# Kernel optimization log

Hardware: AMD Instinct MI355X
Metric: run time of the kernel (lower is better)

Reference implementation:

```python
import jax, jax.numpy as jnp
import numpy as np

NEG_SLOPE = 0.01  # F.leaky_relu default


def gcn_conv(x, W, b, src, dst):
    """PyG GCNConv: add self-loops, symmetric deg^-1/2 normalization, linear, scatter-add."""
    n = x.shape[0]
    loop = jnp.arange(n)
    s = jnp.concatenate([src, loop])  # source j
    d = jnp.concatenate([dst, loop])  # target i
    deg = jax.ops.segment_sum(jnp.ones_like(d, dtype=x.dtype), d, num_segments=n)
    dis = jnp.where(deg > 0, jax.lax.rsqrt(jnp.maximum(deg, 1e-12)), 0.0)
    norm = dis[s] * dis[d]                       # [E+N]
    h = x @ W                                    # [N, out]
    msg = h[s] * norm[:, None]                   # gather + scale
    out = jax.ops.segment_sum(msg, d, num_segments=n)  # scatter-add to targets
    return out + b


def setup_inputs() -> dict:
    key = jax.random.key(0)
    ks = jax.random.split(key, 8)
    N, E, G = 100000, 800000, 100
    IN, H, OUT = 128, 256, 16
    x = jax.random.normal(ks[0], (N, IN), dtype=jnp.float32)
    edge_index = jax.random.randint(ks[1], (2, E), 0, N, dtype=jnp.int64)
    batch = jnp.repeat(jnp.arange(G, dtype=jnp.int64), N // G)  # sorted graph ids
    def glorot(k, fi, fo):
        lim = np.sqrt(6.0 / (fi + fo))
        return jax.random.uniform(k, (fi, fo), jnp.float32, -lim, lim)
    return {
        "x": x, "edge_index": edge_index, "batch": batch,
        "W1": glorot(ks[2], IN, H), "b1": jnp.zeros((H,), jnp.float32),
        "W2": glorot(ks[3], H, H),  "b2": jnp.zeros((H,), jnp.float32),
        "W3": glorot(ks[4], H, OUT), "b3": jnp.zeros((OUT,), jnp.float32),
    }


def reference(x, edge_index, batch, W1, b1, W2, b2, W3, b3):
    src, dst = edge_index[0], edge_index[1]
    h = gcn_conv(x, W1, b1, src, dst)
    h = jax.nn.leaky_relu(h, NEG_SLOPE)  # dropout p=0.0 -> identity
    h = gcn_conv(h, W2, b2, src, dst)
    h = jax.nn.leaky_relu(h, NEG_SLOPE)
    h = gcn_conv(h, W3, b3, src, dst)
    # get_zero_nodes: first node of each graph in the sorted batch vector
    mask = jnp.concatenate([jnp.array([True]), batch[1:] != batch[:-1]])
    return h[mask, :]  # [n_graphs, out_channels]
```

## Files before the change

### kernel.cpp

```cpp
#include <hip/hip_runtime.h>

#define NEG_SLOPE 0.01f

using short8 = __attribute__((ext_vector_type(8))) short;
using f32x4  = __attribute__((ext_vector_type(4))) float;

__device__ inline float b2f(ushort u) {
    union { unsigned u; float f; } x; x.u = ((unsigned)u) << 16; return x.f;
}
__device__ inline ushort f2b(float f) {
    union { float f; unsigned u; } x; x.f = f;
    unsigned r = x.u + 0x7FFFu + ((x.u >> 16) & 1u);
    return (ushort)(r >> 16);
}
__device__ inline void gload16(const void* g, void* l) {
    __builtin_amdgcn_global_load_lds((__attribute__((address_space(1))) void*)g,
                                     (__attribute__((address_space(3))) void*)l, 16, 0, 0);
}


__global__ void count_pick(const int* __restrict__ dst, int* __restrict__ cnt, int E,
                           const int* __restrict__ batch, int* __restrict__ picked,
                           int* __restrict__ rootflag, int N) {
    int i = blockIdx.x * blockDim.x + threadIdx.x;
    if (i < E) atomicAdd(&cnt[dst[i]], 1);
    if (i < N) {
        if (i == 0 || batch[i] != batch[i - 1]) { picked[batch[i]] = i; rootflag[i] = 1; }
    }
}


__global__ void frontier1e(const int* __restrict__ src, const int* __restrict__ dst,
                           const int* __restrict__ rootflag, int* __restrict__ flag1,
                           int E, int N) {
    int i = blockIdx.x * blockDim.x + threadIdx.x;
    if (i < N && rootflag[i]) flag1[i] = 1;
    if (i < E && rootflag[dst[i]]) flag1[src[i]] = 1;
}

__global__ void frontier2e(const int* __restrict__ src, const int* __restrict__ dst,
                           const int* __restrict__ flag1, int* __restrict__ flag2,
                           int E, int N) {
    int i = blockIdx.x * blockDim.x + threadIdx.x;
    if (i < N && flag1[i]) flag2[i] = 1;
    if (i < E && flag1[dst[i]]) flag2[src[i]] = 1;
}


__global__ __launch_bounds__(256) void tscan1(const int* __restrict__ cnt,
                                              const int* __restrict__ f1,
                                              const int* __restrict__ f2,
                                              int4* __restrict__ bsums,
                                              float* __restrict__ dis, int N) {
    __shared__ int l0[256], l1[256], l2[256];
    int b = blockIdx.x, t = threadIdx.x;
    int base = b * 1024 + t * 4;
    int c[4] = {0,0,0,0}, a1[4] = {0,0,0,0}, a2[4] = {0,0,0,0};
    if (base + 3 < N) {
        int4 q = *(const int4*)(cnt + base); c[0]=q.x; c[1]=q.y; c[2]=q.z; c[3]=q.w;
        int4 u = *(const int4*)(f1 + base);  a1[0]=u.x; a1[1]=u.y; a1[2]=u.z; a1[3]=u.w;
        int4 v = *(const int4*)(f2 + base);  a2[0]=v.x; a2[1]=v.y; a2[2]=v.z; a2[3]=v.w;
    } else {
        for (int i = 0; i < 4; i++) if (base + i < N) {
            c[i] = cnt[base + i]; a1[i] = f1[base + i]; a2[i] = f2[base + i];
        }
    }
#pragma unroll
    for (int i = 0; i < 4; i++)
        if (base + i < N) dis[base + i] = rsqrtf((float)c[i] + 1.0f);
    int s0 = 0, s1 = 0, s2 = 0;
#pragma unroll
    for (int i = 0; i < 4; i++) { s0 += a2[i] ? c[i] : 0; s1 += a1[i]; s2 += a2[i]; }
    l0[t] = s0; l1[t] = s1; l2[t] = s2;
    __syncthreads();
    for (int off = 128; off > 0; off >>= 1) {
        if (t < off) { l0[t] += l0[t + off]; l1[t] += l1[t + off]; l2[t] += l2[t + off]; }
        __syncthreads();
    }
    if (t == 0) bsums[b] = make_int4(l0[0], l1[0], l2[0], 0);
}

__global__ __launch_bounds__(1024) void tscan2(int4* __restrict__ bsums, int* __restrict__ counts,
                                               int* __restrict__ rowptr, int N, int nb) {
    __shared__ int l0[1024], l1[1024], l2[1024];
    int t = threadIdx.x;
    int v0 = 0, v1 = 0, v2 = 0;
    if (t < nb) { int4 v = bsums[t]; v0 = v.x; v1 = v.y; v2 = v.z; }
    l0[t] = v0; l1[t] = v1; l2[t] = v2;
    __syncthreads();
    for (int off = 1; off < 1024; off <<= 1) {
        int u0 = (t >= off) ? l0[t - off] : 0;
        int u1 = (t >= off) ? l1[t - off] : 0;
        int u2 = (t >= off) ? l2[t - off] : 0;
        __syncthreads();
        l0[t] += u0; l1[t] += u1; l2[t] += u2;
        __syncthreads();
    }
    if (t < nb) bsums[t] = make_int4(l0[t] - v0, l1[t] - v1, l2[t] - v2, 0);
    if (t == 1023) {
        counts[0] = l1[1023];
        counts[1] = l2[1023];
        rowptr[N] = l0[1023];
    }
}

__global__ __launch_bounds__(256) void tscan3(const int* __restrict__ cnt,
                                              const int* __restrict__ f1,
                                              const int* __restrict__ f2,
                                              const int4* __restrict__ bsums,
                                              int* __restrict__ rowptr, int* __restrict__ cur,
                                              int* __restrict__ pos1, int* __restrict__ pos2,
                                              int* __restrict__ list1, int* __restrict__ list2,
                                              int N) {
    __shared__ int l0[256], l1[256], l2[256];
    int b = blockIdx.x, t = threadIdx.x;
    int base = b * 1024 + t * 4;
    int c[4] = {0,0,0,0}, a1[4] = {0,0,0,0}, a2[4] = {0,0,0,0};
    if (base + 3 < N) {
        int4 q = *(const int4*)(cnt + base); c[0]=q.x; c[1]=q.y; c[2]=q.z; c[3]=q.w;
        int4 u = *(const int4*)(f1 + base);  a1[0]=u.x; a1[1]=u.y; a1[2]=u.z; a1[3]=u.w;
        int4 v = *(const int4*)(f2 + base);  a2[0]=v.x; a2[1]=v.y; a2[2]=v.z; a2[3]=v.w;
    } else {
        for (int i = 0; i < 4; i++) if (base + i < N) {
            c[i] = cnt[base + i]; a1[i] = f1[base + i]; a2[i] = f2[base + i];
        }
    }
    int m[4];
#pragma unroll
    for (int i = 0; i < 4; i++) m[i] = a2[i] ? c[i] : 0;
    int s0 = m[0] + m[1] + m[2] + m[3];
    int s1 = a1[0] + a1[1] + a1[2] + a1[3];
    int s2 = a2[0] + a2[1] + a2[2] + a2[3];
    l0[t] = s0; l1[t] = s1; l2[t] = s2;
    __syncthreads();
    for (int off = 1; off < 256; off <<= 1) {
        int u0 = (t >= off) ? l0[t - off] : 0;
        int u1 = (t >= off) ? l1[t - off] : 0;
        int u2 = (t >= off) ? l2[t - off] : 0;
        __syncthreads();
        l0[t] += u0; l1[t] += u1; l2[t] += u2;
        __syncthreads();
    }
    int4 bs = bsums[b];
    int run0 = bs.x + l0[t] - s0;
    int run1 = bs.y + l1[t] - s1;
    int run2 = bs.z + l2[t] - s2;
#pragma unroll
    for (int i = 0; i < 4; i++) {
        if (base + i < N) {
            rowptr[base + i] = run0;
            cur[base + i] = run0;
            if (a1[i]) { pos1[base + i] = run1; list1[run1] = base + i; }
            if (a2[i]) { pos2[base + i] = run2; list2[run2] = base + i; }
        }
        run0 += m[i]; run1 += a1[i]; run2 += a2[i];
    }
}


__global__ void fill_f(const int* __restrict__ src, const int* __restrict__ dst,
                       const int* __restrict__ flag2, int* __restrict__ cur,
                       int* __restrict__ col, int E) {
    int e = blockIdx.x * blockDim.x + threadIdx.x;
    if (e < E) {
        int d = dst[e];
        if (flag2[d]) {
            int pos = atomicAdd(&cur[d], 1);
            col[pos] = src[e];
        }
    }
}


__global__ void wtrans2(const float* __restrict__ W1, ushort* __restrict__ W1t,
                        const float* __restrict__ W2, ushort* __restrict__ W2t) {
    int idx = blockIdx.x * blockDim.x + threadIdx.x;
    if (idx < 32768) {
        int n = idx >> 7, k = idx & 127;
        W1t[idx] = f2b(W1[k * 256 + n]);
    } else if (idx < 98304) {
        int j = idx - 32768;
        int n = j >> 8, k = j & 255;
        W2t[j] = f2b(W2[k * 256 + n]);
    }
}


__global__ __launch_bounds__(256) void aggx_c(const float* __restrict__ x,
                                              const float* __restrict__ dis,
                                              const int* __restrict__ rowptr,
                                              const int* __restrict__ col,
                                              const int* __restrict__ list2,
                                              const int* __restrict__ counts,
                                              ushort* __restrict__ aggXc) {
    const int M2 = counts[1];
    int wave = blockIdx.x * 4 + (threadIdx.x >> 6);
    int lane = threadIdx.x & 63;
    int li = lane & 31, sub = lane >> 5;
    int stride = gridDim.x * 8;
    const float* xp = x + li * 4;
    for (int p = wave * 2 + sub; p < M2; p += stride) {
        int node = list2[p];
        float di = dis[node];
        float4 sv = *(const float4*)(xp + (size_t)node * 128);
        float a0 = di * sv.x, a1 = di * sv.y, a2 = di * sv.z, a3 = di * sv.w;
        int e1 = rowptr[node + 1];
        for (int e = rowptr[node]; e < e1; e++) {
            int s = col[e];
            float w = dis[s];
            float4 v = *(const float4*)(xp + (size_t)s * 128);
            a0 += w * v.x; a1 += w * v.y; a2 += w * v.z; a3 += w * v.w;
        }
        ushort4 o;
        o.x = f2b(di * a0); o.y = f2b(di * a1); o.z = f2b(di * a2); o.w = f2b(di * a3);
        *(ushort4*)(aggXc + (size_t)p * 128 + li * 4) = o;
    }
}


__global__ __launch_bounds__(256) void agg2_c(const ushort* __restrict__ h1c,
                                              const float* __restrict__ dis,
                                              const int* __restrict__ rowptr,
                                              const int* __restrict__ col,
                                              const int* __restrict__ list1,
                                              const int* __restrict__ pos2,
                                              const int* __restrict__ counts,
                                              ushort* __restrict__ agg1c) {
    const int M1 = counts[0];
    int wave = blockIdx.x * 4 + (threadIdx.x >> 6);
    int lane = threadIdx.x & 63;
    int li = lane & 31, sub = lane >> 5;
    int stride = gridDim.x * 8;
    const ushort* hp = h1c + (size_t)li * 8;
    for (int p = wave * 2 + sub; p < M1; p += stride) {
        int i = list1[p];
        float di = dis[i];
        float a[8];
        {
            short8 v = *(const short8*)(hp + (size_t)pos2[i] * 256);
#pragma unroll
            for (int j = 0; j < 8; j++) a[j] = b2f((ushort)v[j]);
        }
        int e1 = rowptr[i + 1];
        for (int e = rowptr[i]; e < e1; e++) {
            short8 v = *(const short8*)(hp + (size_t)pos2[col[e]] * 256);
#pragma unroll
            for (int j = 0; j < 8; j++) a[j] += b2f((ushort)v[j]);
        }
        short8 o;
#pragma unroll
        for (int j = 0; j < 8; j++) o[j] = (short)f2b(di * a[j]);
        *(short8*)(agg1c + (size_t)p * 256 + li * 8) = o;
    }
}


template <int K>
__global__ __launch_bounds__(512) void gemm_c(const ushort* __restrict__ A,
                                              const ushort* __restrict__ Bt,
                                              const float* __restrict__ bias,
                                              const float* __restrict__ dis,
                                              const int* __restrict__ list,
                                              const int* __restrict__ counts, int which,
                                              ushort* __restrict__ C) {
    __shared__ ushort As[128 * 64];
    __shared__ ushort Bs[256 * 64];
    const int M = counts[which];
    const int t = threadIdx.x;
    const int lane = t & 63;
    const int w = t >> 6;
    const int wm = w >> 2, wn = w & 3;

    for (int tile = blockIdx.x; tile * 128 < M; tile += gridDim.x) {
        const int row0 = tile * 128;
        f32x4 acc[4][4] = {};

        for (int kt = 0; kt < K / 64; kt++) {
#pragma unroll
            for (int it = 0; it < 2; it++) {
                int q = it * 512 + t;
                int r = q >> 3, c = q & 7;
                int cs = c ^ (r & 7);
                int ga = min(row0 + r, M - 1);
                gload16(A + (size_t)ga * K + kt * 64 + cs * 8, &As[q * 8]);
            }
#pragma unroll
            for (int it = 0; it < 4; it++) {
                int q = it * 512 + t;
                int r = q >> 3, c = q & 7;
                int cs = c ^ (r & 7);
                gload16(Bt + (size_t)r * K + kt * 64 + cs * 8, &Bs[q * 8]);
            }
            __syncthreads();
#pragma unroll
            for (int ks = 0; ks < 2; ks++) {
                short8 a[4], b[4];
                int cc = ks * 4 + (lane >> 4);
#pragma unroll
                for (int m = 0; m < 4; m++) {
                    int R = wm * 64 + m * 16 + (lane & 15);
                    a[m] = *(const short8*)&As[R * 64 + ((cc ^ (R & 7)) * 8)];
                }
#pragma unroll
                for (int n = 0; n < 4; n++) {
                    int R = wn * 64 + n * 16 + (lane & 15);
                    b[n] = *(const short8*)&Bs[R * 64 + ((cc ^ (R & 7)) * 8)];
                }
#pragma unroll
                for (int m = 0; m < 4; m++)
#pragma unroll
                    for (int n = 0; n < 4; n++)
                        acc[m][n] = __builtin_amdgcn_mfma_f32_16x16x32_bf16(a[m], b[n], acc[m][n], 0, 0, 0);
            }
            __syncthreads();
        }

#pragma unroll
        for (int m = 0; m < 4; m++) {
#pragma unroll
            for (int j = 0; j < 4; j++) {
                int grow = row0 + wm * 64 + m * 16 + (lane >> 4) * 4 + j;
                if (grow >= M) continue;
                float dr = dis[list[grow]];
#pragma unroll
                for (int n = 0; n < 4; n++) {
                    int gcol = wn * 64 + n * 16 + (lane & 15);
                    float v = acc[m][n][j] + bias[gcol];
                    v = v > 0.f ? v : NEG_SLOPE * v;
                    C[(size_t)grow * 256 + gcol] = f2b(v * dr);
                }
            }
        }
    }
}


__global__ __launch_bounds__(256) void final_c(const ushort* __restrict__ h2c,
                                               const float* __restrict__ dis,
                                               const int* __restrict__ rowptr,
                                               const int* __restrict__ col,
                                               const int* __restrict__ picked,
                                               const int* __restrict__ pos1,
                                               const float* __restrict__ W3,
                                               const float* __restrict__ b3,
                                               float* __restrict__ out, int G) {
    __shared__ float agg[256];
    __shared__ float red[256];
    int g = blockIdx.x;
    int t = threadIdx.x;
    if (g >= G) return;
    int i = picked[g];
    float di = dis[i];
    float a = b2f(h2c[(size_t)pos1[i] * 256 + t]);
    int e1 = rowptr[i + 1];
    for (int e = rowptr[i]; e < e1; e++) {
        a += b2f(h2c[(size_t)pos1[col[e]] * 256 + t]);
    }
    agg[t] = di * a;
    __syncthreads();
    int c = t & 15, seg = t >> 4;
    float p = 0.f;
#pragma unroll
    for (int kk = 0; kk < 16; kk++) {
        int k = seg * 16 + kk;
        p += agg[k] * W3[k * 16 + c];
    }
    red[t] = p;
    __syncthreads();
    if (t < 16) {
        float sres = 0.f;
#pragma unroll
        for (int ss = 0; ss < 16; ss++) sres += red[ss * 16 + t];
        out[g * 16 + t] = sres + b3[t];
    }
}


extern "C" void kernel_launch(void* const* d_in, const int* in_sizes, int n_in,
                              void* d_out, int out_size, void* d_ws, size_t ws_size,
                              hipStream_t stream) {
    const float* x   = (const float*)d_in[0];
    const int* ei    = (const int*)d_in[1];
    const int* batch = (const int*)d_in[2];
    const float* W1  = (const float*)d_in[3];
    const float* b1  = (const float*)d_in[4];
    const float* W2  = (const float*)d_in[5];
    const float* b2  = (const float*)d_in[6];
    const float* W3  = (const float*)d_in[7];
    const float* b3  = (const float*)d_in[8];

    const int IN = 128, H = 256, OUT = 16;
    int N = in_sizes[0] / IN;
    int E = in_sizes[1] / 2;
    int G = out_size / OUT;
    const int* srcp = ei;
    const int* dstp = ei + E;

    char* p = (char*)d_ws;
    auto carve = [&](size_t bytes) {
        char* q = p;
        p += (bytes + 255) & ~(size_t)255;
        return q;
    };
    int*    cnt      = (int*)carve((size_t)N * 4);
    int*    flag1    = (int*)carve((size_t)N * 4);
    int*    flag2    = (int*)carve((size_t)N * 4);
    int*    rootflag = (int*)carve((size_t)N * 4);
    char*   zend     = p;
    float*  dis    = (float*)carve((size_t)N * 4);
    int*    rowptr = (int*)carve(((size_t)N + 1) * 4);
    int*    cur    = (int*)carve((size_t)N * 4);
    int4*   tbsums = (int4*)carve(1024 * 16);
    int*    counts = (int*)carve(256);
    int*    picked = (int*)carve((size_t)G * 4);
    int*    pos1   = (int*)carve((size_t)N * 4);
    int*    pos2   = (int*)carve((size_t)N * 4);
    int*    list1  = (int*)carve((size_t)N * 4);
    int*    list2  = (int*)carve((size_t)N * 4);
    int*    col    = (int*)carve((size_t)E * 4);
    ushort* W1t    = (ushort*)carve((size_t)256 * 128 * 2);
    ushort* W2t    = (ushort*)carve((size_t)256 * 256 * 2);
    ushort* RA     = (ushort*)carve((size_t)N * H * 2);
    ushort* RB     = (ushort*)carve((size_t)N * H * 2);

    ushort* aggXc = RA;
    ushort* agg1c = RA;
    ushort* h1c   = RB;
    ushort* h2c   = RB;

    int nb = (N + 1023) / 1024;
    int cpN = (E > N ? E : N);

    hipMemsetAsync(cnt, 0, (size_t)(zend - (char*)cnt), stream);

    count_pick<<<(cpN + 255) / 256, 256, 0, stream>>>(dstp, cnt, E, batch, picked, rootflag, N);

    frontier1e<<<(cpN + 255) / 256, 256, 0, stream>>>(srcp, dstp, rootflag, flag1, E, N);
    frontier2e<<<(cpN + 255) / 256, 256, 0, stream>>>(srcp, dstp, flag1, flag2, E, N);

    tscan1<<<nb, 256, 0, stream>>>(cnt, flag1, flag2, tbsums, dis, N);
    tscan2<<<1, 1024, 0, stream>>>(tbsums, counts, rowptr, N, nb);
    tscan3<<<nb, 256, 0, stream>>>(cnt, flag1, flag2, tbsums, rowptr, cur, pos1, pos2, list1, list2, N);

    fill_f<<<(E + 255) / 256, 256, 0, stream>>>(srcp, dstp, flag2, cur, col, E);

    wtrans2<<<(98304 + 255) / 256, 256, 0, stream>>>(W1, W1t, W2, W2t);

    aggx_c<<<512, 256, 0, stream>>>(x, dis, rowptr, col, list2, counts, aggXc);
    gemm_c<128><<<256, 512, 0, stream>>>(aggXc, W1t, b1, dis, list2, counts, 1, h1c);

    agg2_c<<<128, 256, 0, stream>>>(h1c, dis, rowptr, col, list1, pos2, counts, agg1c);
    gemm_c<256><<<64, 512, 0, stream>>>(agg1c, W2t, b2, dis, list1, counts, 0, h2c);

    final_c<<<G, 256, 0, stream>>>(h2c, dis, rowptr, col, picked, pos1, W3, b3, (float*)d_out, G);
}
```

Baseline: 146.3 us.

## Fuse preprocessing kernels, vectorize edge passes, unroll gather loop

Replaces the memset with an init kernel and merges degree counting into the first frontier pass. The frontier and CSR-fill kernels now read four edges per thread with int4 loads. The weight transpose is folded into the first scan kernel. The aggregation loop is unrolled by two and its grid doubled. Together these cut kernel launches and raise memory-level parallelism in the graph preprocessing stages. The cost is extra grid-stride work in the scan kernel and a wider but less balanced per-thread edge load.

```diff
diff --git a/kernel.cpp b/kernel.cpp
--- a/kernel.cpp
+++ b/kernel.cpp
@@ -19,65 +19,116 @@
 }
 
 
-__global__ void count_pick(const int* __restrict__ dst, int* __restrict__ cnt, int E,
-                           const int* __restrict__ batch, int* __restrict__ picked,
-                           int* __restrict__ rootflag, int N) {
+__global__ void init_kernel(const int* __restrict__ batch, int* __restrict__ cnt,
+                            int* __restrict__ flag1, int* __restrict__ flag2,
+                            int* __restrict__ rootflag, int* __restrict__ picked, int N) {
     int i = blockIdx.x * blockDim.x + threadIdx.x;
-    if (i < E) atomicAdd(&cnt[dst[i]], 1);
-    if (i < N) {
-        if (i == 0 || batch[i] != batch[i - 1]) { picked[batch[i]] = i; rootflag[i] = 1; }
-    }
-}
-
-
-__global__ void frontier1e(const int* __restrict__ src, const int* __restrict__ dst,
-                           const int* __restrict__ rootflag, int* __restrict__ flag1,
-                           int E, int N) {
+    if (i >= N) return;
+    cnt[i] = 0;
+    int root = (i == 0) || (batch[i] != batch[i - 1]);
+    flag1[i] = root;
+    flag2[i] = 0;
+    rootflag[i] = root;
+    if (root) picked[batch[i]] = i;
+}
+
+
+__global__ void count_f1(const int* __restrict__ src, const int* __restrict__ dst,
+                         const int* __restrict__ rootflag, int* __restrict__ cnt,
+                         int* __restrict__ flag1, int E) {
     int i = blockIdx.x * blockDim.x + threadIdx.x;
-    if (i < N && rootflag[i]) flag1[i] = 1;
-    if (i < E && rootflag[dst[i]]) flag1[src[i]] = 1;
-}
-
-__global__ void frontier2e(const int* __restrict__ src, const int* __restrict__ dst,
+    int e0 = i * 4;
+    if (e0 + 3 < E) {
+        int4 dq = *(const int4*)(dst + e0);
+        int r0 = rootflag[dq.x], r1 = rootflag[dq.y], r2 = rootflag[dq.z], r3 = rootflag[dq.w];
+        atomicAdd(&cnt[dq.x], 1);
+        atomicAdd(&cnt[dq.y], 1);
+        atomicAdd(&cnt[dq.z], 1);
+        atomicAdd(&cnt[dq.w], 1);
+        if (r0 | r1 | r2 | r3) {
+            int4 sq = *(const int4*)(src + e0);
+            if (r0) flag1[sq.x] = 1;
+            if (r1) flag1[sq.y] = 1;
+            if (r2) flag1[sq.z] = 1;
+            if (r3) flag1[sq.w] = 1;
+        }
+    } else if (e0 < E) {
+        for (int e = e0; e < E; e++) {
+            int d = dst[e];
+            atomicAdd(&cnt[d], 1);
+            if (rootflag[d]) flag1[src[e]] = 1;
+        }
+    }
+}
+
+
+__global__ void frontier2v(const int* __restrict__ src, const int* __restrict__ dst,
                            const int* __restrict__ flag1, int* __restrict__ flag2,
                            int E, int N) {
     int i = blockIdx.x * blockDim.x + threadIdx.x;
+    int e0 = i * 4;
+    if (e0 + 3 < E) {
+        int4 dq = *(const int4*)(dst + e0);
+        int f0 = flag1[dq.x], f1 = flag1[dq.y], f2 = flag1[dq.z], f3 = flag1[dq.w];
+        if (f0 | f1 | f2 | f3) {
+            int4 sq = *(const int4*)(src + e0);
+            if (f0) flag2[sq.x] = 1;
+            if (f1) flag2[sq.y] = 1;
+            if (f2) flag2[sq.z] = 1;
+            if (f3) flag2[sq.w] = 1;
+        }
+    } else if (e0 < E) {
+        for (int e = e0; e < E; e++) if (flag1[dst[e]]) flag2[src[e]] = 1;
+    }
     if (i < N && flag1[i]) flag2[i] = 1;
-    if (i < E && flag1[dst[i]]) flag2[src[i]] = 1;
-}
-
-
-__global__ __launch_bounds__(256) void tscan1(const int* __restrict__ cnt,
-                                              const int* __restrict__ f1,
-                                              const int* __restrict__ f2,
-                                              int4* __restrict__ bsums,
-                                              float* __restrict__ dis, int N) {
+}
+
+
+__global__ __launch_bounds__(256) void tscan1w(const int* __restrict__ cnt,
+                                               const int* __restrict__ f1,
+                                               const int* __restrict__ f2,
+                                               int4* __restrict__ bsums,
+                                               float* __restrict__ dis, int N, int nb,
+                                               const float* __restrict__ W1, ushort* __restrict__ W1t,
+                                               const float* __restrict__ W2, ushort* __restrict__ W2t) {
     __shared__ int l0[256], l1[256], l2[256];
     int b = blockIdx.x, t = threadIdx.x;
-    int base = b * 1024 + t * 4;
-    int c[4] = {0,0,0,0}, a1[4] = {0,0,0,0}, a2[4] = {0,0,0,0};
-    if (base + 3 < N) {
-        int4 q = *(const int4*)(cnt + base); c[0]=q.x; c[1]=q.y; c[2]=q.z; c[3]=q.w;
-        int4 u = *(const int4*)(f1 + base);  a1[0]=u.x; a1[1]=u.y; a1[2]=u.z; a1[3]=u.w;
-        int4 v = *(const int4*)(f2 + base);  a2[0]=v.x; a2[1]=v.y; a2[2]=v.z; a2[3]=v.w;
-    } else {
-        for (int i = 0; i < 4; i++) if (base + i < N) {
-            c[i] = cnt[base + i]; a1[i] = f1[base + i]; a2[i] = f2[base + i];
-        }
-    }
-#pragma unroll
-    for (int i = 0; i < 4; i++)
-        if (base + i < N) dis[base + i] = rsqrtf((float)c[i] + 1.0f);
-    int s0 = 0, s1 = 0, s2 = 0;
-#pragma unroll
-    for (int i = 0; i < 4; i++) { s0 += a2[i] ? c[i] : 0; s1 += a1[i]; s2 += a2[i]; }
-    l0[t] = s0; l1[t] = s1; l2[t] = s2;
-    __syncthreads();
-    for (int off = 128; off > 0; off >>= 1) {
-        if (t < off) { l0[t] += l0[t + off]; l1[t] += l1[t + off]; l2[t] += l2[t + off]; }
+    if (b < nb) {
+        int base = b * 1024 + t * 4;
+        int c[4] = {0,0,0,0}, a1[4] = {0,0,0,0}, a2[4] = {0,0,0,0};
+        if (base + 3 < N) {
+            int4 q = *(const int4*)(cnt + base); c[0]=q.x; c[1]=q.y; c[2]=q.z; c[3]=q.w;
+            int4 u = *(const int4*)(f1 + base);  a1[0]=u.x; a1[1]=u.y; a1[2]=u.z; a1[3]=u.w;
+            int4 v = *(const int4*)(f2 + base);  a2[0]=v.x; a2[1]=v.y; a2[2]=v.z; a2[3]=v.w;
+        } else {
+            for (int i = 0; i < 4; i++) if (base + i < N) {
+                c[i] = cnt[base + i]; a1[i] = f1[base + i]; a2[i] = f2[base + i];
+            }
+        }
+#pragma unroll
+        for (int i = 0; i < 4; i++)
+            if (base + i < N) dis[base + i] = rsqrtf((float)c[i] + 1.0f);
+        int s0 = 0, s1 = 0, s2 = 0;
+#pragma unroll
+        for (int i = 0; i < 4; i++) { s0 += a2[i] ? c[i] : 0; s1 += a1[i]; s2 += a2[i]; }
+        l0[t] = s0; l1[t] = s1; l2[t] = s2;
         __syncthreads();
-    }
-    if (t == 0) bsums[b] = make_int4(l0[0], l1[0], l2[0], 0);
+        for (int off = 128; off > 0; off >>= 1) {
+            if (t < off) { l0[t] += l0[t + off]; l1[t] += l1[t + off]; l2[t] += l2[t + off]; }
+            __syncthreads();
+        }
+        if (t == 0) bsums[b] = make_int4(l0[0], l1[0], l2[0], 0);
+    }
+    for (int idx = b * 256 + t; idx < 98304; idx += gridDim.x * 256) {
+        if (idx < 32768) {
+            int n = idx >> 7, k = idx & 127;
+            W1t[idx] = f2b(W1[k * 256 + n]);
+        } else {
+            int j = idx - 32768;
+            int n = j >> 8, k = j & 255;
+            W2t[j] = f2b(W2[k * 256 + n]);
+        }
+    }
 }
 
 __global__ __launch_bounds__(1024) void tscan2(int4* __restrict__ bsums, int* __restrict__ counts,
@@ -158,30 +209,26 @@
 }
 
 
-__global__ void fill_f(const int* __restrict__ src, const int* __restrict__ dst,
-                       const int* __restrict__ flag2, int* __restrict__ cur,
-                       int* __restrict__ col, int E) {
-    int e = blockIdx.x * blockDim.x + threadIdx.x;
-    if (e < E) {
-        int d = dst[e];
-        if (flag2[d]) {
-            int pos = atomicAdd(&cur[d], 1);
-            col[pos] = src[e];
-        }
-    }
-}
-
-
-__global__ void wtrans2(const float* __restrict__ W1, ushort* __restrict__ W1t,
-                        const float* __restrict__ W2, ushort* __restrict__ W2t) {
-    int idx = blockIdx.x * blockDim.x + threadIdx.x;
-    if (idx < 32768) {
-        int n = idx >> 7, k = idx & 127;
-        W1t[idx] = f2b(W1[k * 256 + n]);
-    } else if (idx < 98304) {
-        int j = idx - 32768;
-        int n = j >> 8, k = j & 255;
-        W2t[j] = f2b(W2[k * 256 + n]);
+__global__ void fill_fv(const int* __restrict__ src, const int* __restrict__ dst,
+                        const int* __restrict__ flag2, int* __restrict__ cur,
+                        int* __restrict__ col, int E) {
+    int i = blockIdx.x * blockDim.x + threadIdx.x;
+    int e0 = i * 4;
+    if (e0 + 3 < E) {
+        int4 dq = *(const int4*)(dst + e0);
+        int f0 = flag2[dq.x], f1 = flag2[dq.y], f2 = flag2[dq.z], f3 = flag2[dq.w];
+        if (f0 | f1 | f2 | f3) {
+            int4 sq = *(const int4*)(src + e0);
+            if (f0) col[atomicAdd(&cur[dq.x], 1)] = sq.x;
+            if (f1) col[atomicAdd(&cur[dq.y], 1)] = sq.y;
+            if (f2) col[atomicAdd(&cur[dq.z], 1)] = sq.z;
+            if (f3) col[atomicAdd(&cur[dq.w], 1)] = sq.w;
+        }
+    } else if (e0 < E) {
+        for (int e = e0; e < E; e++) {
+            int d = dst[e];
+            if (flag2[d]) col[atomicAdd(&cur[d], 1)] = src[e];
+        }
     }
 }
 
@@ -204,8 +251,18 @@
         float di = dis[node];
         float4 sv = *(const float4*)(xp + (size_t)node * 128);
         float a0 = di * sv.x, a1 = di * sv.y, a2 = di * sv.z, a3 = di * sv.w;
-        int e1 = rowptr[node + 1];
-        for (int e = rowptr[node]; e < e1; e++) {
+        int e = rowptr[node], e1 = rowptr[node + 1];
+        for (; e + 2 <= e1; e += 2) {
+            int s0 = col[e], s1 = col[e + 1];
+            float w0 = dis[s0], w1 = dis[s1];
+            float4 v0 = *(const float4*)(xp + (size_t)s0 * 128);
+            float4 v1 = *(const float4*)(xp + (size_t)s1 * 128);
+            a0 += w0 * v0.x + w1 * v1.x;
+            a1 += w0 * v0.y + w1 * v1.y;
+            a2 += w0 * v0.z + w1 * v1.z;
+            a3 += w0 * v0.w + w1 * v1.w;
+        }
+        if (e < e1) {
             int s = col[e];
             float w = dis[s];
             float4 v = *(const float4*)(xp + (size_t)s * 128);
@@ -406,7 +463,6 @@
     int*    flag1    = (int*)carve((size_t)N * 4);
     int*    flag2    = (int*)carve((size_t)N * 4);
     int*    rootflag = (int*)carve((size_t)N * 4);
-    char*   zend     = p;
     float*  dis    = (float*)carve((size_t)N * 4);
     int*    rowptr = (int*)carve(((size_t)N + 1) * 4);
     int*    cur    = (int*)carve((size_t)N * 4);
@@ -429,24 +485,23 @@
     ushort* h2c   = RB;
 
     int nb = (N + 1023) / 1024;
-    int cpN = (E > N ? E : N);
-
-    hipMemsetAsync(cnt, 0, (size_t)(zend - (char*)cnt), stream);
-
-    count_pick<<<(cpN + 255) / 256, 256, 0, stream>>>(dstp, cnt, E, batch, picked, rootflag, N);
-
-    frontier1e<<<(cpN + 255) / 256, 256, 0, stream>>>(srcp, dstp, rootflag, flag1, E, N);
-    frontier2e<<<(cpN + 255) / 256, 256, 0, stream>>>(srcp, dstp, flag1, flag2, E, N);
-
-    tscan1<<<nb, 256, 0, stream>>>(cnt, flag1, flag2, tbsums, dis, N);
+    int e4 = (E + 3) / 4;
+    int epN = (e4 > N ? e4 : N);
+    int scanw_grid = (nb > 384 ? nb : 384);
+
+    init_kernel<<<(N + 255) / 256, 256, 0, stream>>>(batch, cnt, flag1, flag2, rootflag, picked, N);
+
+    count_f1<<<(e4 + 255) / 256, 256, 0, stream>>>(srcp, dstp, rootflag, cnt, flag1, E);
+
+    frontier2v<<<(epN + 255) / 256, 256, 0, stream>>>(srcp, dstp, flag1, flag2, E, N);
+
+    tscan1w<<<scanw_grid, 256, 0, stream>>>(cnt, flag1, flag2, tbsums, dis, N, nb, W1, W1t, W2, W2t);
     tscan2<<<1, 1024, 0, stream>>>(tbsums, counts, rowptr, N, nb);
     tscan3<<<nb, 256, 0, stream>>>(cnt, flag1, flag2, tbsums, rowptr, cur, pos1, pos2, list1, list2, N);
 
-    fill_f<<<(E + 255) / 256, 256, 0, stream>>>(srcp, dstp, flag2, cur, col, E);
-
-    wtrans2<<<(98304 + 255) / 256, 256, 0, stream>>>(W1, W1t, W2, W2t);
-
-    aggx_c<<<512, 256, 0, stream>>>(x, dis, rowptr, col, list2, counts, aggXc);
+    fill_fv<<<(e4 + 255) / 256, 256, 0, stream>>>(srcp, dstp, flag2, cur, col, E);
+
+    aggx_c<<<1024, 256, 0, stream>>>(x, dis, rowptr, col, list2, counts, aggXc);
     gemm_c<128><<<256, 512, 0, stream>>>(aggXc, W1t, b1, dis, list2, counts, 1, h1c);
 
     agg2_c<<<128, 256, 0, stream>>>(h1c, dis, rowptr, col, list1, pos2, counts, agg1c);
```

Result: faster. 134.1 us (-8.3%).
